# Performance work log

Measured on AMD Instinct MI355X. Metric: run time of the kernel, lower is better.

Reference implementation:

```python
import jax, jax.numpy as jnp
import numpy as np
from jax import lax

SCALE = 2
K_UP = 5
BN_EPS = 1e-5
DN = ('NCHW', 'OIHW', 'NCHW')


def bn_eval(x, gamma, beta):
    # BatchNorm2d in eval mode with running_mean=0, running_var=1
    s = gamma / jnp.sqrt(1.0 + BN_EPS)
    return x * s[None, :, None, None] + beta[None, :, None, None]


def pixel_shuffle(x, r):
    b, C, h, w = x.shape
    c = C // (r * r)
    x = x.reshape(b, c, r, r, h, w)
    x = x.transpose(0, 1, 4, 2, 5, 3)  # b, c, h, r, w, r
    return x.reshape(b, c, h * r, w * r)


def setup_inputs() -> dict:
    key = jax.random.key(0)
    ks = jax.random.split(key, 3)
    b, c, h, w = 4, 128, 64, 64
    c_mid = 64
    return {
        'X': jax.random.normal(ks[0], (b, c, h, w), dtype=jnp.float32),
        'comp_w': jax.random.normal(ks[1], (c_mid, c, 1, 1), dtype=jnp.float32) * 0.05,
        'comp_g': jnp.ones((c_mid,), jnp.float32),
        'comp_b': jnp.zeros((c_mid,), jnp.float32),
        'enc_w': jax.random.normal(ks[2], ((SCALE * K_UP) ** 2, c_mid, 3, 3), dtype=jnp.float32) * 0.05,
        'enc_g': jnp.ones(((SCALE * K_UP) ** 2,), jnp.float32),
        'enc_b': jnp.zeros(((SCALE * K_UP) ** 2,), jnp.float32),
    }


def reference(X, comp_w, comp_g, comp_b, enc_w, enc_g, enc_b):
    b, c, h, w = X.shape
    h_, w_ = h * SCALE, w * SCALE
    pad = K_UP // 2 * SCALE  # = 4

    # comp: 1x1 conv + BN + SiLU
    W = lax.conv_general_dilated(X, comp_w, (1, 1), [(0, 0), (0, 0)], dimension_numbers=DN)
    W = jax.nn.silu(bn_eval(W, comp_g, comp_b))
    # enc: 3x3 conv (pad 1) + BN, no activation
    W = lax.conv_general_dilated(W, enc_w, (1, 1), [(1, 1), (1, 1)], dimension_numbers=DN)
    W = bn_eval(W, enc_g, enc_b)
    # pixel shuffle -> [b, k_up^2, h_, w_], softmax over kernel dim
    W = pixel_shuffle(W, SCALE)
    W = jax.nn.softmax(W, axis=1)

    # nearest-neighbor upsample of X
    Xu = jnp.repeat(jnp.repeat(X, SCALE, axis=2), SCALE, axis=3)  # [b, c, h_, w_]
    # unfold: kernel k_up, dilation=scale, padding=pad (im2col, channel-major)
    P = lax.conv_general_dilated_patches(
        Xu, (K_UP, K_UP), (1, 1), [(pad, pad), (pad, pad)],
        rhs_dilation=(SCALE, SCALE), dimension_numbers=DN)  # [b, c*k^2, h_, w_]
    P = P.reshape(b, c, K_UP * K_UP, h_, w_)

    return jnp.einsum('bkhw,bckhw->bchw', W, P)
```

## Files before the change

kernel.cpp:

```cpp
#include <hip/hip_runtime.h>
#include <hip/hip_bf16.h>
#include <math.h>

#define Bn   4
#define CIN  128
#define Hh   64
#define Ww   64
#define HW   4096
#define CMID 64
#define KOC  100
#define H2   128
#define W2d  128
#define HW2  16384
#define KUP  5
#define BN_EPS 1e-5f
#define CCH  8

typedef __attribute__((ext_vector_type(4)))  short  short4v;
typedef __attribute__((ext_vector_type(8)))  short  short8v;
typedef __attribute__((ext_vector_type(16))) float  float16v;

__device__ __forceinline__ ushort f2bf(float v) {
    __hip_bfloat16 h = __float2bfloat16(v);
    return *(ushort*)&h;
}

__global__ __launch_bounds__(256) void comp_kernel(
    const float* __restrict__ X,
    const float* __restrict__ cw,
    const float* __restrict__ cg,
    const float* __restrict__ cb,
    const float* __restrict__ ew,
    ushort* __restrict__ W1b,
    ushort* __restrict__ Abf)
{
    __shared__ float cwS[64 * 129];

    int tid = threadIdx.x;
    int blk = blockIdx.x;

    for (int i = tid; i < 64 * 128; i += 256) {
        int co_s = i >> 7, ci_s = i & 127;
        cwS[co_s * 129 + ci_s] = cw[i];
    }

    if (blk < 288) {
        int i   = blk * 256 + tid;
        int cm  = i & 63;
        int kop = (i >> 6) & 127;
        int tap = i >> 13;
        float v = (kop < KOC) ? ew[((size_t)(kop * CMID + cm)) * 9 + tap] : 0.f;
        Abf[i] = f2bf(v);
    }
    __syncthreads();

    int b   = blk >> 8;
    int pix = ((blk & 255) << 4) + ((tid >> 6) << 2);
    int co  = tid & 63;

    const float* xb = X + (size_t)b * CIN * HW + pix;
    const float* wrow = cwS + co * 129;
    float a0 = 0.f, a1 = 0.f, a2 = 0.f, a3 = 0.f;

#pragma unroll 4
    for (int ci = 0; ci < CIN; ++ci) {
        float4 xv = *(const float4*)(xb + (size_t)ci * HW);
        float w = wrow[ci];
        a0 += xv.x * w; a1 += xv.y * w; a2 += xv.z * w; a3 += xv.w * w;
    }

    float inv_s = rsqrtf(1.0f + BN_EPS);
    float s0 = cg[co] * inv_s, bb0 = cb[co];
    float r[4] = {a0, a1, a2, a3};
    ushort* wp = W1b + ((size_t)b * HW + pix) * 64 + co;
#pragma unroll
    for (int i = 0; i < 4; ++i) {
        float v = r[i] * s0 + bb0;
        v = v / (1.f + expf(-v));
        wp[(size_t)i * 64] = f2bf(v);
    }
}

__global__ __launch_bounds__(256) void enc_kernel(
    const ushort* __restrict__ W1b_us,
    const ushort* __restrict__ Abf,
    const float* __restrict__ eg,
    const float* __restrict__ eb,
    float* __restrict__ Wsm)
{
    __shared__ ushort Bs[3 * 34 * 72];
    __shared__ float  redm[4][8][32];
    __shared__ float  reds[4][8][32];

    int bid   = blockIdx.x;
    int whalf = bid & 1;
    int h     = (bid >> 1) & 63;
    int b     = bid >> 7;
    int w0    = whalf * 32;
    int tid   = threadIdx.x;

    const unsigned* src  = (const unsigned*)W1b_us;
    unsigned*       dstu = (unsigned*)Bs;
    for (int i = tid; i < 3 * 34 * 32; i += 256) {
        int cp = i & 31;
        int t  = i >> 5;
        int wl = t % 34;
        int r  = t / 34;
        int gr = h - 1 + r, gw = w0 - 1 + wl;
        unsigned val = 0u;
        if ((unsigned)gr < 64u && (unsigned)gw < 64u)
            val = src[((size_t)b * HW + gr * 64 + gw) * 32 + cp];
        dstu[(r * 34 + wl) * 36 + cp] = val;
    }
    __syncthreads();

    int lane = tid & 63;
    int wid  = tid >> 6;
    int n    = lane & 31;
    int q    = lane >> 5;

    float16v acc;
#pragma unroll
    for (int i = 0; i < 16; ++i) acc[i] = 0.f;

    const ushort* Arow = Abf + ((size_t)(wid * 32 + n)) * 64 + q * 8;

#pragma unroll
    for (int tap = 0; tap < 9; ++tap) {
        int dy = tap / 3, dx = tap % 3;
        int bbase = ((dy * 34) + n + dx) * 72 + q * 8;
        const ushort* Atap = Arow + (size_t)tap * 128 * 64;
#pragma unroll
        for (int c = 0; c < 4; ++c) {
            short8v a = *(const short8v*)(Atap + c * 16);
            short8v bf = *(const short8v*)(Bs + bbase + c * 16);
            acc = __builtin_amdgcn_mfma_f32_32x32x16_bf16(a, bf, acc, 0, 0, 0);
        }
    }

    float inv_s = rsqrtf(1.0f + BN_EPS);
    int   widq  = wid * 2 + q;

    float v[16];
    float pmax[4] = {-1e30f, -1e30f, -1e30f, -1e30f};
#pragma unroll
    for (int g = 0; g < 4; ++g) {
        int base = wid * 32 + 8 * g + 4 * q;
        if (base < KOC) {
            float4 gg = *(const float4*)(eg + base);
            float4 bb = *(const float4*)(eb + base);
            float v0 = acc[4*g+0] * (gg.x * inv_s) + bb.x;
            float v1 = acc[4*g+1] * (gg.y * inv_s) + bb.y;
            float v2 = acc[4*g+2] * (gg.z * inv_s) + bb.z;
            float v3 = acc[4*g+3] * (gg.w * inv_s) + bb.w;
            v[4*g+0] = v0; v[4*g+1] = v1; v[4*g+2] = v2; v[4*g+3] = v3;
            pmax[0] = fmaxf(pmax[0], v0);
            pmax[1] = fmaxf(pmax[1], v1);
            pmax[2] = fmaxf(pmax[2], v2);
            pmax[3] = fmaxf(pmax[3], v3);
        } else {
            v[4*g+0] = -1e30f; v[4*g+1] = -1e30f;
            v[4*g+2] = -1e30f; v[4*g+3] = -1e30f;
        }
    }

#pragma unroll
    for (int j = 0; j < 4; ++j) redm[j][widq][n] = pmax[j];
    __syncthreads();
    float m[4];
#pragma unroll
    for (int j = 0; j < 4; ++j) {
        float mm = redm[j][0][n];
#pragma unroll
        for (int i = 1; i < 8; ++i) mm = fmaxf(mm, redm[j][i][n]);
        m[j] = mm;
    }

    float psum[4] = {0.f, 0.f, 0.f, 0.f};
#pragma unroll
    for (int g = 0; g < 4; ++g) {
#pragma unroll
        for (int j = 0; j < 4; ++j) {
            float e = expf(v[4*g+j] - m[j]);
            v[4*g+j] = e;
            psum[j] += e;
        }
    }
#pragma unroll
    for (int j = 0; j < 4; ++j) reds[j][widq][n] = psum[j];
    __syncthreads();
    float inv[4];
#pragma unroll
    for (int j = 0; j < 4; ++j) {
        float ss = reds[j][0][n];
#pragma unroll
        for (int i = 1; i < 8; ++i) ss += reds[j][i][n];
        inv[j] = 1.f / ss;
    }

    int pixn = h * 64 + w0 + n;
    float* Wp = Wsm + (size_t)b * KOC * HW + pixn;
#pragma unroll
    for (int reg = 0; reg < 16; ++reg) {
        int row = (reg & 3) + 8 * (reg >> 2) + 4 * q;
        int ko  = wid * 32 + row;
        if (ko < KOC) Wp[(size_t)ko * HW] = v[reg] * inv[reg & 3];
    }
}

__global__ __launch_bounds__(256) void carafe_kernel(
    const float* __restrict__ X,
    const float* __restrict__ Wsm,
    float* __restrict__ out)
{
    int gt = blockIdx.x * blockDim.x + threadIdx.x;
    int w  = gt & 63;
    int h  = (gt >> 6) & 63;
    int b  = (gt >> 12) & 3;
    int chunk = gt >> 14;
    int c0 = chunk * CCH;
    int pix = h * Ww + w;

    float wt[100];
    const float* wpb = Wsm + (size_t)b * KOC * HW + pix;
#pragma unroll
    for (int k = 0; k < 25; ++k) {
        wt[k]      = wpb[(size_t)(4 * k + 0) * HW];
        wt[25 + k] = wpb[(size_t)(4 * k + 1) * HW];
        wt[50 + k] = wpb[(size_t)(4 * k + 2) * HW];
        wt[75 + k] = wpb[(size_t)(4 * k + 3) * HW];
    }

    int off[25];
#pragma unroll
    for (int ki = 0; ki < 5; ++ki) {
#pragma unroll
        for (int kj = 0; kj < 5; ++kj) {
            int k = ki * 5 + kj;
            int r = h + ki - 2, cc = w + kj - 2;
            bool valid = ((unsigned)r < 64u) && ((unsigned)cc < 64u);
            int rc = r < 0 ? 0 : (r > 63 ? 63 : r);
            int cx = cc < 0 ? 0 : (cc > 63 ? 63 : cc);
            off[k] = rc * Ww + cx;
            if (!valid) { wt[k] = 0.f; wt[25+k] = 0.f; wt[50+k] = 0.f; wt[75+k] = 0.f; }
        }
    }

    const float* xp = X + ((size_t)b * CIN + c0) * HW;
    float* o0 = out + ((size_t)b * CIN + c0) * HW2 + (2 * h) * W2d + 2 * w;

    for (int c = 0; c < CCH; ++c) {
        float x[25];
#pragma unroll
        for (int k = 0; k < 25; ++k) x[k] = xp[off[k]];
        float a0 = 0.f, a1 = 0.f, a2 = 0.f, a3 = 0.f;
#pragma unroll
        for (int k = 0; k < 25; ++k) {
            float xv = x[k];
            a0 += wt[k]      * xv;
            a1 += wt[25 + k] * xv;
            a2 += wt[50 + k] * xv;
            a3 += wt[75 + k] * xv;
        }
        *(float2*)o0          = make_float2(a0, a1);
        *(float2*)(o0 + W2d)  = make_float2(a2, a3);
        xp += HW;
        o0 += HW2;
    }
}

extern "C" void kernel_launch(void* const* d_in, const int* in_sizes, int n_in,
                              void* d_out, int out_size, void* d_ws, size_t ws_size,
                              hipStream_t stream)
{
    const float* X  = (const float*)d_in[0];
    const float* cw = (const float*)d_in[1];
    const float* cg = (const float*)d_in[2];
    const float* cb = (const float*)d_in[3];
    const float* ew = (const float*)d_in[4];
    const float* eg = (const float*)d_in[5];
    const float* eb = (const float*)d_in[6];
    float* out = (float*)d_out;

    char* ws = (char*)d_ws;
    ushort* W1b = (ushort*)ws;
    ushort* Abf = (ushort*)(ws + 2097152);
    float*  Wsm = (float*)(ws + 2097152 + 147456);

    comp_kernel  <<<1024, 256, 0, stream>>>(X, cw, cg, cb, ew, W1b, Abf);
    enc_kernel   <<<512, 256, 0, stream>>>(W1b, Abf, eg, eb, Wsm);
    carafe_kernel<<<16 * Bn * HW / 256, 256, 0, stream>>>(X, Wsm, out);
}
```

Measured before the change: 128.1 us.

## Fuse encoder softmax with CARAFE reassembly through shared memory

```diff
diff --git a/kernel.cpp b/kernel.cpp
--- a/kernel.cpp
+++ b/kernel.cpp
@@ -14,7 +14,6 @@
 #define HW2  16384
 #define KUP  5
 #define BN_EPS 1e-5f
-#define CCH  8
 
 typedef __attribute__((ext_vector_type(4)))  short  short4v;
 typedef __attribute__((ext_vector_type(8)))  short  short8v;
@@ -81,16 +80,20 @@
     }
 }
 
-__global__ __launch_bounds__(256) void enc_kernel(
+__global__ __launch_bounds__(256) void enc_carafe_kernel(
     const ushort* __restrict__ W1b_us,
     const ushort* __restrict__ Abf,
     const float* __restrict__ eg,
     const float* __restrict__ eb,
-    float* __restrict__ Wsm)
+    const float* __restrict__ X,
+    float* __restrict__ out)
 {
-    __shared__ ushort Bs[3 * 34 * 72];
-    __shared__ float  redm[4][8][32];
-    __shared__ float  reds[4][8][32];
+    __shared__ __align__(16) char smem[22880];
+    ushort* Bs   = (ushort*)smem;
+    float*  redm = (float*)(smem + 14688);
+    float*  reds = (float*)(smem + 18784);
+    float*  wsL  = (float*)smem;
+    float*  xs   = (float*)(smem + 12800);
 
     int bid   = blockIdx.x;
     int whalf = bid & 1;
@@ -165,14 +168,14 @@
     }
 
 #pragma unroll
-    for (int j = 0; j < 4; ++j) redm[j][widq][n] = pmax[j];
+    for (int j = 0; j < 4; ++j) redm[(j * 8 + widq) * 32 + n] = pmax[j];
     __syncthreads();
     float m[4];
 #pragma unroll
     for (int j = 0; j < 4; ++j) {
-        float mm = redm[j][0][n];
-#pragma unroll
-        for (int i = 1; i < 8; ++i) mm = fmaxf(mm, redm[j][i][n]);
+        float mm = redm[(j * 8 + 0) * 32 + n];
+#pragma unroll
+        for (int i = 1; i < 8; ++i) mm = fmaxf(mm, redm[(j * 8 + i) * 32 + n]);
         m[j] = mm;
     }
 
@@ -187,51 +190,37 @@
         }
     }
 #pragma unroll
-    for (int j = 0; j < 4; ++j) reds[j][widq][n] = psum[j];
+    for (int j = 0; j < 4; ++j) reds[(j * 8 + widq) * 32 + n] = psum[j];
     __syncthreads();
     float inv[4];
 #pragma unroll
     for (int j = 0; j < 4; ++j) {
-        float ss = reds[j][0][n];
-#pragma unroll
-        for (int i = 1; i < 8; ++i) ss += reds[j][i][n];
+        float ss = reds[(j * 8 + 0) * 32 + n];
+#pragma unroll
+        for (int i = 1; i < 8; ++i) ss += reds[(j * 8 + i) * 32 + n];
         inv[j] = 1.f / ss;
     }
-
-    int pixn = h * 64 + w0 + n;
-    float* Wp = Wsm + (size_t)b * KOC * HW + pixn;
+    __syncthreads();
+
 #pragma unroll
     for (int reg = 0; reg < 16; ++reg) {
         int row = (reg & 3) + 8 * (reg >> 2) + 4 * q;
         int ko  = wid * 32 + row;
-        if (ko < KOC) Wp[(size_t)ko * HW] = v[reg] * inv[reg & 3];
-    }
-}
-
-__global__ __launch_bounds__(256) void carafe_kernel(
-    const float* __restrict__ X,
-    const float* __restrict__ Wsm,
-    float* __restrict__ out)
-{
-    int gt = blockIdx.x * blockDim.x + threadIdx.x;
-    int w  = gt & 63;
-    int h  = (gt >> 6) & 63;
-    int b  = (gt >> 12) & 3;
-    int chunk = gt >> 14;
-    int c0 = chunk * CCH;
-    int pix = h * Ww + w;
+        if (ko < KOC) wsL[ko * 32 + n] = v[reg] * inv[reg & 3];
+    }
+    __syncthreads();
+
+    int p = tid & 31;
+    int s = tid >> 5;
+    int w = w0 + p;
 
     float wt[100];
-    const float* wpb = Wsm + (size_t)b * KOC * HW + pix;
 #pragma unroll
     for (int k = 0; k < 25; ++k) {
-        wt[k]      = wpb[(size_t)(4 * k + 0) * HW];
-        wt[25 + k] = wpb[(size_t)(4 * k + 1) * HW];
-        wt[50 + k] = wpb[(size_t)(4 * k + 2) * HW];
-        wt[75 + k] = wpb[(size_t)(4 * k + 3) * HW];
-    }
-
-    int off[25];
+#pragma unroll
+        for (int j = 0; j < 4; ++j)
+            wt[j * 25 + k] = wsL[(4 * k + j) * 32 + p];
+    }
 #pragma unroll
     for (int ki = 0; ki < 5; ++ki) {
 #pragma unroll
@@ -239,33 +228,43 @@
             int k = ki * 5 + kj;
             int r = h + ki - 2, cc = w + kj - 2;
             bool valid = ((unsigned)r < 64u) && ((unsigned)cc < 64u);
-            int rc = r < 0 ? 0 : (r > 63 ? 63 : r);
-            int cx = cc < 0 ? 0 : (cc > 63 ? 63 : cc);
-            off[k] = rc * Ww + cx;
             if (!valid) { wt[k] = 0.f; wt[25+k] = 0.f; wt[50+k] = 0.f; wt[75+k] = 0.f; }
         }
     }
 
-    const float* xp = X + ((size_t)b * CIN + c0) * HW;
-    float* o0 = out + ((size_t)b * CIN + c0) * HW2 + (2 * h) * W2d + 2 * w;
-
-    for (int c = 0; c < CCH; ++c) {
-        float x[25];
-#pragma unroll
-        for (int k = 0; k < 25; ++k) x[k] = xp[off[k]];
+    const int sbase = s * 180;
+    for (int g = 0; g < 16; ++g) {
+        __syncthreads();
+        for (int i = tid; i < 8 * 5 * 36; i += 256) {
+            int cs  = i / 180;
+            int rem = i - cs * 180;
+            int r   = rem / 36;
+            int col = rem - r * 36;
+            int gr  = h - 2 + r;
+            int rc  = gr < 0 ? 0 : (gr > 63 ? 63 : gr);
+            int gcol = w0 - 2 + col;
+            int gcc  = gcol < 0 ? 0 : (gcol > 63 ? 63 : gcol);
+            xs[i] = X[((size_t)b * CIN + (g * 8 + cs)) * HW + rc * 64 + gcc];
+        }
+        __syncthreads();
+
+        int c = g * 8 + s;
         float a0 = 0.f, a1 = 0.f, a2 = 0.f, a3 = 0.f;
 #pragma unroll
-        for (int k = 0; k < 25; ++k) {
-            float xv = x[k];
-            a0 += wt[k]      * xv;
-            a1 += wt[25 + k] * xv;
-            a2 += wt[50 + k] * xv;
-            a3 += wt[75 + k] * xv;
-        }
-        *(float2*)o0          = make_float2(a0, a1);
-        *(float2*)(o0 + W2d)  = make_float2(a2, a3);
-        xp += HW;
-        o0 += HW2;
+        for (int ki = 0; ki < 5; ++ki) {
+#pragma unroll
+            for (int kj = 0; kj < 5; ++kj) {
+                int k = ki * 5 + kj;
+                float xv = xs[sbase + ki * 36 + p + kj];
+                a0 += wt[k]      * xv;
+                a1 += wt[25 + k] * xv;
+                a2 += wt[50 + k] * xv;
+                a3 += wt[75 + k] * xv;
+            }
+        }
+        float* o = out + ((size_t)b * CIN + c) * HW2 + (size_t)(2 * h) * W2d + 2 * w;
+        *(float2*)o         = make_float2(a0, a1);
+        *(float2*)(o + W2d) = make_float2(a2, a3);
     }
 }
 
@@ -285,9 +284,7 @@
     char* ws = (char*)d_ws;
     ushort* W1b = (ushort*)ws;
     ushort* Abf = (ushort*)(ws + 2097152);
-    float*  Wsm = (float*)(ws + 2097152 + 147456);
-
-    comp_kernel  <<<1024, 256, 0, stream>>>(X, cw, cg, cb, ew, W1b, Abf);
-    enc_kernel   <<<512, 256, 0, stream>>>(W1b, Abf, eg, eb, Wsm);
-    carafe_kernel<<<16 * Bn * HW / 256, 256, 0, stream>>>(X, Wsm, out);
-}
+
+    comp_kernel      <<<1024, 256, 0, stream>>>(X, cw, cg, cb, ew, W1b, Abf);
+    enc_carafe_kernel<<<512, 256, 0, stream>>>(W1b, Abf, eg, eb, X, out);
+}
```

Measured after the change: 149.8 us. 1.17x slower.

## Stage X tile in LDS and compute 2 channels x 4 pixels per thread in comp_kernel

Applied to the files above, without the earlier changes.

```diff
diff --git a/kernel.cpp b/kernel.cpp
--- a/kernel.cpp
+++ b/kernel.cpp
@@ -34,18 +34,27 @@
     ushort* __restrict__ W1b,
     ushort* __restrict__ Abf)
 {
-    __shared__ float cwS[64 * 129];
-
-    int tid = threadIdx.x;
-    int blk = blockIdx.x;
-
-    for (int i = tid; i < 64 * 128; i += 256) {
-        int co_s = i >> 7, ci_s = i & 127;
-        cwS[co_s * 129 + ci_s] = cw[i];
-    }
-
-    if (blk < 288) {
-        int i   = blk * 256 + tid;
+    __shared__ float xsS[128 * 32];
+    __shared__ float cwT[128 * 66];
+
+    int tid  = threadIdx.x;
+    int blk  = blockIdx.x;
+    int b    = blk >> 7;
+    int pix0 = (blk & 127) * 32;
+
+    const float* xb = X + (size_t)b * CIN * HW + pix0;
+
+    for (int s = tid; s < 1024; s += 256) {
+        int ci = s >> 3, seg = s & 7;
+        *(float4*)&xsS[ci * 32 + seg * 4] =
+            *(const float4*)(xb + (size_t)ci * HW + seg * 4);
+    }
+    for (int i = tid; i < 8192; i += 256) {
+        int co = i >> 7, ci = i & 127;
+        cwT[ci * 66 + co] = cw[i];
+    }
+    for (int t = tid; t < 144; t += 256) {
+        int i   = blk * 144 + t;
         int cm  = i & 63;
         int kop = (i >> 6) & 127;
         int tap = i >> 13;
@@ -54,30 +63,34 @@
     }
     __syncthreads();
 
-    int b   = blk >> 8;
-    int pix = ((blk & 255) << 4) + ((tid >> 6) << 2);
-    int co  = tid & 63;
-
-    const float* xb = X + (size_t)b * CIN * HW + pix;
-    const float* wrow = cwS + co * 129;
-    float a0 = 0.f, a1 = 0.f, a2 = 0.f, a3 = 0.f;
+    int px4 = (tid & 7) * 4;
+    int co2 = (tid >> 3) * 2;
+
+    float a00 = 0.f, a01 = 0.f, a02 = 0.f, a03 = 0.f;
+    float a10 = 0.f, a11 = 0.f, a12 = 0.f, a13 = 0.f;
 
 #pragma unroll 4
-    for (int ci = 0; ci < CIN; ++ci) {
-        float4 xv = *(const float4*)(xb + (size_t)ci * HW);
-        float w = wrow[ci];
-        a0 += xv.x * w; a1 += xv.y * w; a2 += xv.z * w; a3 += xv.w * w;
+    for (int ci = 0; ci < 128; ++ci) {
+        float4 xv = *(const float4*)&xsS[ci * 32 + px4];
+        float2 wv = *(const float2*)&cwT[ci * 66 + co2];
+        a00 += xv.x * wv.x; a01 += xv.y * wv.x;
+        a02 += xv.z * wv.x; a03 += xv.w * wv.x;
+        a10 += xv.x * wv.y; a11 += xv.y * wv.y;
+        a12 += xv.z * wv.y; a13 += xv.w * wv.y;
     }
 
     float inv_s = rsqrtf(1.0f + BN_EPS);
-    float s0 = cg[co] * inv_s, bb0 = cb[co];
-    float r[4] = {a0, a1, a2, a3};
-    ushort* wp = W1b + ((size_t)b * HW + pix) * 64 + co;
+    float s0 = cg[co2] * inv_s,     bb0 = cb[co2];
+    float s1 = cg[co2 + 1] * inv_s, bb1 = cb[co2 + 1];
+    float r0[4] = {a00, a01, a02, a03};
+    float r1[4] = {a10, a11, a12, a13};
+    unsigned* wp = (unsigned*)W1b + ((size_t)b * HW + pix0 + px4) * 32 + (co2 >> 1);
 #pragma unroll
     for (int i = 0; i < 4; ++i) {
-        float v = r[i] * s0 + bb0;
-        v = v / (1.f + expf(-v));
-        wp[(size_t)i * 64] = f2bf(v);
+        float v0 = r0[i] * s0 + bb0; v0 = v0 / (1.f + expf(-v0));
+        float v1 = r1[i] * s1 + bb1; v1 = v1 / (1.f + expf(-v1));
+        unsigned pk = (unsigned)f2bf(v0) | ((unsigned)f2bf(v1) << 16);
+        wp[(size_t)i * 32] = pk;
     }
 }
 
@@ -287,7 +300,7 @@
     ushort* Abf = (ushort*)(ws + 2097152);
     float*  Wsm = (float*)(ws + 2097152 + 147456);
 
-    comp_kernel  <<<1024, 256, 0, stream>>>(X, cw, cg, cb, ew, W1b, Abf);
+    comp_kernel  <<<512, 256, 0, stream>>>(X, cw, cg, cb, ew, W1b, Abf);
     enc_kernel   <<<512, 256, 0, stream>>>(W1b, Abf, eg, eb, Wsm);
     carafe_kernel<<<16 * Bn * HW / 256, 256, 0, stream>>>(X, Wsm, out);
 }
```

Result: faster. 117.7 us (-8.1%).

## Rewrite 1x1 comp conv as split-bf16 MFMA GEMM with larger tiles

Applied to the files above, without the earlier changes.

```diff
diff --git a/kernel.cpp b/kernel.cpp
--- a/kernel.cpp
+++ b/kernel.cpp
@@ -15,6 +15,7 @@
 #define KUP  5
 #define BN_EPS 1e-5f
 #define CCH  8
+#define LDP  136
 
 typedef __attribute__((ext_vector_type(4)))  short  short4v;
 typedef __attribute__((ext_vector_type(8)))  short  short8v;
@@ -23,6 +24,10 @@
 __device__ __forceinline__ ushort f2bf(float v) {
     __hip_bfloat16 h = __float2bfloat16(v);
     return *(ushort*)&h;
+}
+__device__ __forceinline__ float bfbits2f(ushort u) {
+    unsigned x = ((unsigned)u) << 16;
+    return __uint_as_float(x);
 }
 
 __global__ __launch_bounds__(256) void comp_kernel(
@@ -34,50 +39,91 @@
     ushort* __restrict__ W1b,
     ushort* __restrict__ Abf)
 {
-    __shared__ float cwS[64 * 129];
-
-    int tid = threadIdx.x;
-    int blk = blockIdx.x;
-
-    for (int i = tid; i < 64 * 128; i += 256) {
-        int co_s = i >> 7, ci_s = i & 127;
-        cwS[co_s * 129 + ci_s] = cw[i];
-    }
-
-    if (blk < 288) {
-        int i   = blk * 256 + tid;
+    extern __shared__ __align__(16) char dsm[];
+    ushort* AsH = (ushort*)dsm;
+    ushort* AsL = AsH + 64 * LDP;
+    ushort* XsH = AsL + 64 * LDP;
+    ushort* XsL = XsH + 64 * LDP;
+
+    int tid  = threadIdx.x;
+    int blk  = blockIdx.x;
+    int b    = blk >> 6;
+    int pix0 = (blk & 63) * 64;
+
+    for (int t = tid; t < 288; t += 256) {
+        int i   = blk * 288 + t;
         int cm  = i & 63;
         int kop = (i >> 6) & 127;
         int tap = i >> 13;
         float v = (kop < KOC) ? ew[((size_t)(kop * CMID + cm)) * 9 + tap] : 0.f;
         Abf[i] = f2bf(v);
     }
+    for (int i = tid; i < 8192; i += 256) {
+        int co = i >> 7, ci = i & 127;
+        float x  = cw[i];
+        ushort h = f2bf(x);
+        ushort l = f2bf(x - bfbits2f(h));
+        AsH[co * LDP + ci] = h;
+        AsL[co * LDP + ci] = l;
+    }
+    const float* xb = X + (size_t)b * CIN * HW + pix0;
+    for (int i = tid; i < 8192; i += 256) {
+        int p = i & 63, ci = i >> 6;
+        float x  = xb[(size_t)ci * HW + p];
+        ushort h = f2bf(x);
+        ushort l = f2bf(x - bfbits2f(h));
+        XsH[p * LDP + ci] = h;
+        XsL[p * LDP + ci] = l;
+    }
     __syncthreads();
 
-    int b   = blk >> 8;
-    int pix = ((blk & 255) << 4) + ((tid >> 6) << 2);
-    int co  = tid & 63;
-
-    const float* xb = X + (size_t)b * CIN * HW + pix;
-    const float* wrow = cwS + co * 129;
-    float a0 = 0.f, a1 = 0.f, a2 = 0.f, a3 = 0.f;
-
-#pragma unroll 4
-    for (int ci = 0; ci < CIN; ++ci) {
-        float4 xv = *(const float4*)(xb + (size_t)ci * HW);
-        float w = wrow[ci];
-        a0 += xv.x * w; a1 += xv.y * w; a2 += xv.z * w; a3 += xv.w * w;
+    int lane = tid & 63;
+    int wid  = tid >> 6;
+    int n    = lane & 31;
+    int q    = lane >> 5;
+    int h2   = wid >> 1;
+    int p2   = wid & 1;
+
+    float16v acc;
+#pragma unroll
+    for (int i = 0; i < 16; ++i) acc[i] = 0.f;
+
+    const ushort* aH = AsH + (h2 * 32 + n) * LDP + q * 8;
+    const ushort* aL = AsL + (h2 * 32 + n) * LDP + q * 8;
+    const ushort* xH = XsH + (p2 * 32 + n) * LDP + q * 8;
+    const ushort* xL = XsL + (p2 * 32 + n) * LDP + q * 8;
+
+#pragma unroll
+    for (int c = 0; c < 8; ++c) {
+        short8v ah = *(const short8v*)(aH + c * 16);
+        short8v al = *(const short8v*)(aL + c * 16);
+        short8v bh = *(const short8v*)(xH + c * 16);
+        short8v bl = *(const short8v*)(xL + c * 16);
+        acc = __builtin_amdgcn_mfma_f32_32x32x16_bf16(ah, bh, acc, 0, 0, 0);
+        acc = __builtin_amdgcn_mfma_f32_32x32x16_bf16(ah, bl, acc, 0, 0, 0);
+        acc = __builtin_amdgcn_mfma_f32_32x32x16_bf16(al, bh, acc, 0, 0, 0);
     }
 
     float inv_s = rsqrtf(1.0f + BN_EPS);
-    float s0 = cg[co] * inv_s, bb0 = cb[co];
-    float r[4] = {a0, a1, a2, a3};
-    ushort* wp = W1b + ((size_t)b * HW + pix) * 64 + co;
-#pragma unroll
-    for (int i = 0; i < 4; ++i) {
-        float v = r[i] * s0 + bb0;
-        v = v / (1.f + expf(-v));
-        wp[(size_t)i * 64] = f2bf(v);
+    int pixa = pix0 + p2 * 32 + n;
+    ushort* wp = W1b + ((size_t)b * HW + pixa) * 64;
+#pragma unroll
+    for (int g = 0; g < 4; ++g) {
+        int base = h2 * 32 + 8 * g + 4 * q;
+        float4 gg = *(const float4*)(cg + base);
+        float4 bb = *(const float4*)(cb + base);
+        float v0 = acc[4*g+0] * (gg.x * inv_s) + bb.x;
+        float v1 = acc[4*g+1] * (gg.y * inv_s) + bb.y;
+        float v2 = acc[4*g+2] * (gg.z * inv_s) + bb.z;
+        float v3 = acc[4*g+3] * (gg.w * inv_s) + bb.w;
+        v0 = v0 / (1.f + expf(-v0));
+        v1 = v1 / (1.f + expf(-v1));
+        v2 = v2 / (1.f + expf(-v2));
+        v3 = v3 / (1.f + expf(-v3));
+        short4v pk;
+        pk[0] = (short)f2bf(v0); pk[1] = (short)f2bf(v1);
+        pk[2] = (short)f2bf(v2); pk[3] = (short)f2bf(v3);
+        *(short4v*)(wp + base) = pk;
     }
 }
 
@@ -287,7 +333,7 @@
     ushort* Abf = (ushort*)(ws + 2097152);
     float*  Wsm = (float*)(ws + 2097152 + 147456);
 
-    comp_kernel  <<<1024, 256, 0, stream>>>(X, cw, cg, cb, ew, W1b, Abf);
+    comp_kernel  <<<256, 256, 4 * 64 * LDP * 2, stream>>>(X, cw, cg, cb, ew, W1b, Abf);
     enc_kernel   <<<512, 256, 0, stream>>>(W1b, Abf, eg, eb, Wsm);
     carafe_kernel<<<16 * Bn * HW / 256, 256, 0, stream>>>(X, Wsm, out);
 }
```

Measured after the change: 119.5 us. -6.7%, faster.
